# Performance work log

Hardware: AMD Instinct MI355X
Metric: run time of the kernel (lower is better)

Reference implementation:

```python
import jax, jax.numpy as jnp
import numpy as np

N_NODES = 100000
N_EDGES = 1600000
EDGE_FEAT = 16
EDGE_HID = 32
NODE_FEAT = 128


def setup_inputs() -> dict:
    key = jax.random.key(0)
    ks = jax.random.split(key, 10)
    inp = {
        "edge_logits": jax.random.normal(ks[0], (N_EDGES, 1), dtype=jnp.float32),
        "edge_feats": jax.random.normal(ks[1], (N_EDGES, EDGE_FEAT), dtype=jnp.float32),
        "node_feats": jax.random.normal(ks[2], (N_NODES, NODE_FEAT), dtype=jnp.float32),
        "dst": jax.random.randint(ks[3], (N_EDGES,), 0, N_NODES, dtype=jnp.int32),
        # edge_transform Linear(edge_feat -> edge_hid)
        "W_et": jax.random.normal(ks[4], (EDGE_FEAT, EDGE_HID), dtype=jnp.float32) * (1.0 / np.sqrt(EDGE_FEAT)),
        "b_et": jnp.zeros((EDGE_HID,), dtype=jnp.float32),
        # MLP Linear(edge_hid + node_feat -> node_feat)
        "W1": jax.random.normal(ks[5], (EDGE_HID + NODE_FEAT, NODE_FEAT), dtype=jnp.float32) * (1.0 / np.sqrt(EDGE_HID + NODE_FEAT)),
        "b1": jnp.zeros((NODE_FEAT,), dtype=jnp.float32),
        # MLP Linear(node_feat -> node_feat)
        "W2": jax.random.normal(ks[6], (NODE_FEAT, NODE_FEAT), dtype=jnp.float32) * (1.0 / np.sqrt(NODE_FEAT)),
        "b2": jnp.zeros((NODE_FEAT,), dtype=jnp.float32),
    }
    return inp


def reference(edge_logits, edge_feats, node_feats, dst, W_et, b_et, W1, b1, W2, b2):
    # edge_softmax: segment softmax of edge_logits grouped by destination node
    logits = edge_logits[:, 0]                                        # [E]
    seg_max = jax.ops.segment_max(logits, dst, num_segments=N_NODES)  # [N]
    seg_max = jnp.where(jnp.isfinite(seg_max), seg_max, 0.0)          # guard empty segments
    ex = jnp.exp(logits - seg_max[dst])                               # [E]
    denom = jax.ops.segment_sum(ex, dst, num_segments=N_NODES)        # [N]
    denom = jnp.where(denom == 0.0, 1.0, denom)
    alpha = ex / denom[dst]                                           # [E]
    # edge transform (dropout is identity in eval) then weight by attention
    e = alpha[:, None] * (edge_feats @ W_et + b_et)                   # [E, H]
    # scatter-sum aggregation to destination nodes
    c = jax.ops.segment_sum(e, dst, num_segments=N_NODES)             # [N, H]
    context = jax.nn.elu(c)
    h = jnp.concatenate([context, node_feats], axis=1)                # [N, H+F]
    h = jax.nn.relu(h @ W1 + b1)
    return jax.nn.relu(h @ W2 + b2)                                   # [N, F]
```

## Files before the change

### kernel.cpp

```cpp
#include <hip/hip_runtime.h>

#define EF 16
#define EH 32
#define NF 128
#define K1 160
#define HS 168
#define H2S 136

typedef __attribute__((ext_vector_type(8))) short bf16x8;
typedef __attribute__((ext_vector_type(4))) float f32x4;

__device__ __forceinline__ unsigned short f2b(float f) {
  unsigned u = __float_as_uint(f);
  u += 0x7FFFu + ((u >> 16) & 1u);
  return (unsigned short)(u >> 16);
}

__global__ void k_init(unsigned* __restrict__ cnt, int n,
                       const float* __restrict__ W1, const float* __restrict__ W2,
                       unsigned short* __restrict__ w1t, unsigned short* __restrict__ w2t) {
  int i = blockIdx.x * blockDim.x + threadIdx.x;
  if (i < n) cnt[i] = 0u;
  if (i < K1 * NF) {
    int nn = i / K1, k = i % K1;
    w1t[i] = f2b(W1[k * NF + nn]);
  } else if (i < K1 * NF + NF * NF) {
    int j = i - K1 * NF;
    int nn = j / NF, k = j % NF;
    w2t[j] = f2b(W2[k * NF + nn]);
  }
}

__global__ void k_hist(const int* __restrict__ dst, unsigned* __restrict__ cnt, int n_edges) {
  int e = blockIdx.x * blockDim.x + threadIdx.x;
  if (e >= n_edges) return;
  atomicAdd(&cnt[dst[e]], 1u);
}

__global__ void k_scan1(const unsigned* __restrict__ cnt, unsigned* __restrict__ offs,
                        unsigned* __restrict__ bsum, int n) {
  __shared__ unsigned ts[256];
  int t = threadIdx.x;
  int base = blockIdx.x * 1024 + t * 4;
  unsigned v[4];
#pragma unroll
  for (int i = 0; i < 4; ++i) { int idx = base + i; v[i] = (idx < n) ? cnt[idx] : 0u; }
  unsigned run = 0;
#pragma unroll
  for (int i = 0; i < 4; ++i) { unsigned x = v[i]; v[i] = run; run += x; }
  ts[t] = run;
  __syncthreads();
  for (int off = 1; off < 256; off <<= 1) {
    unsigned add = (t >= off) ? ts[t - off] : 0u;
    __syncthreads();
    ts[t] += add;
    __syncthreads();
  }
  unsigned texcl = (t > 0) ? ts[t - 1] : 0u;
  if (t == 255) bsum[blockIdx.x] = ts[255];
#pragma unroll
  for (int i = 0; i < 4; ++i) { int idx = base + i; if (idx < n) offs[idx] = v[i] + texcl; }
}

__global__ void k_scan3(unsigned* __restrict__ offs, unsigned* __restrict__ cursor,
                        const unsigned* __restrict__ bsum, int n, int nb) {
  __shared__ unsigned ts[256];
  int t = threadIdx.x;
  ts[t] = (t < nb) ? bsum[t] : 0u;
  __syncthreads();
  for (int off = 1; off < 256; off <<= 1) {
    unsigned add = (t >= off) ? ts[t - off] : 0u;
    __syncthreads();
    ts[t] += add;
    __syncthreads();
  }
  unsigned add = (blockIdx.x > 0) ? ts[blockIdx.x - 1] : 0u;
  int base = blockIdx.x * 1024 + t * 4;
#pragma unroll
  for (int i = 0; i < 4; ++i) {
    int idx = base + i;
    if (idx < n) { unsigned v = offs[idx] + add; offs[idx] = v; cursor[idx] = v; }
  }
}

__global__ __launch_bounds__(256) void k_perm(
    const int* __restrict__ dst, const float* __restrict__ logits,
    unsigned* __restrict__ cursor, uint2* __restrict__ perm,
    int n_edges, int n_nodes, int chunks) {
  int xcd = blockIdx.x & 7;
  int chunk = blockIdx.x >> 3;
  int lo = (int)((long long)n_nodes * xcd >> 3);
  int hi = (int)((long long)n_nodes * (xcd + 1) >> 3);
  int per = (n_edges + chunks - 1) / chunks;
  int e0 = chunk * per;
  int e1 = min(e0 + per, n_edges);
  for (int e = e0 + (int)threadIdx.x; e < e1; e += 256) {
    int d = __builtin_nontemporal_load(&dst[e]);
    if (d >= lo && d < hi) {
      unsigned slot = atomicAdd(&cursor[d], 1u);
      float ex = __expf(__builtin_nontemporal_load(&logits[e]));
      perm[slot] = make_uint2((unsigned)e, __float_as_uint(ex));
    }
  }
}

__global__ __launch_bounds__(256) void k_gather(
    const uint2* __restrict__ perm, const float* __restrict__ efeat,
    const unsigned* __restrict__ cnt, const unsigned* __restrict__ offs,
    const float* __restrict__ W_et, const float* __restrict__ b_et,
    unsigned short* __restrict__ ctxb, int n_nodes) {
  int node = (int)((blockIdx.x * blockDim.x + threadIdx.x) >> 6);
  if (node >= n_nodes) return;
  int lane = threadIdx.x & 63;
  unsigned start = offs[node];
  unsigned deg = cnt[node];
  int g = lane >> 4, c = lane & 15;
  float a = 0.0f, dsum = 0.0f;
  for (unsigned i = g; i < deg; i += 4) {
    uint2 rec = perm[start + i];
    float ex = __uint_as_float(rec.y);
    float f = efeat[(size_t)rec.x * EF + c];
    a += ex * f;
    dsum += ex;
  }
  a += __shfl_xor(a, 16);      a += __shfl_xor(a, 32);
  dsum += __shfl_xor(dsum, 16); dsum += __shfl_xor(dsum, 32);
  float inv = (deg > 0) ? 1.0f / dsum : 0.0f;
  float S = (deg > 0) ? 1.0f : 0.0f;
  int j = lane & 31;
  float acc = 0.0f;
#pragma unroll
  for (int k = 0; k < 16; ++k) {
    float sk = __shfl(a, k);
    acc += sk * W_et[k * EH + j];
  }
  float cv = acc * inv + S * b_et[j];
  float ctxv = (cv > 0.0f) ? cv : (__expf(cv) - 1.0f);
  if (lane < 32) ctxb[(size_t)node * EH + lane] = f2b(ctxv);
}

__global__ __launch_bounds__(256) void k_node(
    const unsigned short* __restrict__ ctxb, const float* __restrict__ nf,
    const unsigned short* __restrict__ w1t, const unsigned short* __restrict__ w2t,
    const float* __restrict__ b1, const float* __restrict__ b2,
    float* __restrict__ out, int n_nodes) {
  __shared__ __align__(16) unsigned short hA[64 * HS];
  __shared__ __align__(16) unsigned short hB[64 * H2S];
  const int t = threadIdx.x;
  const int w = t >> 6, lane = t & 63;
  const int m = lane & 15, q = lane >> 4;
  int n0 = blockIdx.x * 64;
  if (n0 + 64 > n_nodes) n0 = n_nodes - 64;

  {
    int node = t >> 2, j = (t & 3) * 8;
    *(uint4*)&hA[node * HS + j] = *(const uint4*)&ctxb[(size_t)(n0 + node) * EH + j];
  }
#pragma unroll
  for (int i = 0; i < 8; ++i) {
    int idx = t + 256 * i;
    int node = idx >> 5, j = (idx & 31) * 4;
    float4 v = *(const float4*)&nf[(size_t)(n0 + node) * NF + j];
    unsigned short r[4] = {f2b(v.x), f2b(v.y), f2b(v.z), f2b(v.w)};
    *(uint2*)&hA[node * HS + EH + j] = *(const uint2*)r;
  }
  __syncthreads();

  const int mr = w * 16;
  f32x4 acc[8];
#pragma unroll
  for (int nt = 0; nt < 8; ++nt) acc[nt] = (f32x4){0.f, 0.f, 0.f, 0.f};
  for (int ks = 0; ks < 5; ++ks) {
    bf16x8 a = *(const bf16x8*)&hA[(mr + m) * HS + ks * 32 + q * 8];
#pragma unroll
    for (int nt = 0; nt < 8; ++nt) {
      bf16x8 b = *(const bf16x8*)&w1t[(size_t)(nt * 16 + m) * K1 + ks * 32 + q * 8];
      acc[nt] = __builtin_amdgcn_mfma_f32_16x16x32_bf16(a, b, acc[nt], 0, 0, 0);
    }
  }
#pragma unroll
  for (int nt = 0; nt < 8; ++nt) {
    float bb = b1[nt * 16 + m];
#pragma unroll
    for (int r = 0; r < 4; ++r) {
      float v = fmaxf(acc[nt][r] + bb, 0.0f);
      hB[(mr + q * 4 + r) * H2S + nt * 16 + m] = f2b(v);
    }
  }
  __syncthreads();

  f32x4 ac2[8];
#pragma unroll
  for (int nt = 0; nt < 8; ++nt) ac2[nt] = (f32x4){0.f, 0.f, 0.f, 0.f};
  for (int ks = 0; ks < 4; ++ks) {
    bf16x8 a = *(const bf16x8*)&hB[(mr + m) * H2S + ks * 32 + q * 8];
#pragma unroll
    for (int nt = 0; nt < 8; ++nt) {
      bf16x8 b = *(const bf16x8*)&w2t[(size_t)(nt * 16 + m) * NF + ks * 32 + q * 8];
      ac2[nt] = __builtin_amdgcn_mfma_f32_16x16x32_bf16(a, b, ac2[nt], 0, 0, 0);
    }
  }
#pragma unroll
  for (int nt = 0; nt < 8; ++nt) {
    float bb = b2[nt * 16 + m];
#pragma unroll
    for (int r = 0; r < 4; ++r) {
      out[(size_t)(n0 + mr + q * 4 + r) * NF + nt * 16 + m] = fmaxf(ac2[nt][r] + bb, 0.0f);
    }
  }
}

extern "C" void kernel_launch(void* const* d_in, const int* in_sizes, int n_in,
                              void* d_out, int out_size, void* d_ws, size_t ws_size,
                              hipStream_t stream) {
  const float* edge_logits = (const float*)d_in[0];
  const float* edge_feats  = (const float*)d_in[1];
  const float* node_feats  = (const float*)d_in[2];
  const int*   dst         = (const int*)d_in[3];
  const float* W_et        = (const float*)d_in[4];
  const float* b_et        = (const float*)d_in[5];
  const float* W1          = (const float*)d_in[6];
  const float* b1          = (const float*)d_in[7];
  const float* W2          = (const float*)d_in[8];
  const float* b2          = (const float*)d_in[9];
  float* out = (float*)d_out;

  const int E = in_sizes[0];
  const int n = in_sizes[2] / NF;

  unsigned* cnt    = (unsigned*)d_ws;
  unsigned* offs   = cnt + n;
  unsigned* cursor = offs + n;
  unsigned* bsum   = cursor + n;
  uint2* perm = (uint2*)(((uintptr_t)(bsum + 256) + 255) & ~(uintptr_t)255);
  unsigned short* ctxb = (unsigned short*)(perm + E);
  unsigned short* w1t  = ctxb + (size_t)n * EH;
  unsigned short* w2t  = w1t + NF * K1;

  const int thr = 256;
  const int nscan = (n + 1023) / 1024;
  const int chunks = 256;

  k_init<<<(n + thr - 1) / thr, thr, 0, stream>>>(cnt, n, W1, W2, w1t, w2t);
  k_hist<<<(E + thr - 1) / thr, thr, 0, stream>>>(dst, cnt, E);
  k_scan1<<<nscan, 256, 0, stream>>>(cnt, offs, bsum, n);
  k_scan3<<<nscan, 256, 0, stream>>>(offs, cursor, bsum, n, nscan);
  k_perm<<<chunks * 8, 256, 0, stream>>>(dst, edge_logits, cursor, perm, E, n, chunks);
  k_gather<<<(n * 64 + thr - 1) / thr, thr, 0, stream>>>(perm, edge_feats, cnt, offs,
                                                         W_et, b_et, ctxb, n);
  k_node<<<(n + 63) / 64, 256, 0, stream>>>(ctxb, node_feats, w1t, w2t, b1, b2, out, n);
}
```

Before: 470.7 us.

## Record histogram ranks to drop perm atomics; XCD-aware gather with unrolled loads

The histogram kernel now stores each edge's atomic return value as its rank within its destination bucket. The permutation kernel then computes the slot as offs[d]+rank[e] instead of doing a second atomicAdd on a cursor array, which also removes the cursor array. The gather kernel maps blocks to node ranges per XCD so that perm writes and reads land on the same XCD's L2, and unrolls the edge loop four-way with nontemporal feature loads to raise memory-level parallelism. The cost is an extra 6.4 MB write and read of the rank array.

```diff
diff --git a/kernel.cpp b/kernel.cpp
--- a/kernel.cpp
+++ b/kernel.cpp
@@ -31,10 +31,11 @@
   }
 }
 
-__global__ void k_hist(const int* __restrict__ dst, unsigned* __restrict__ cnt, int n_edges) {
+__global__ void k_hist(const int* __restrict__ dst, unsigned* __restrict__ cnt,
+                       unsigned* __restrict__ rank, int n_edges) {
   int e = blockIdx.x * blockDim.x + threadIdx.x;
   if (e >= n_edges) return;
-  atomicAdd(&cnt[dst[e]], 1u);
+  rank[e] = atomicAdd(&cnt[dst[e]], 1u);
 }
 
 __global__ void k_scan1(const unsigned* __restrict__ cnt, unsigned* __restrict__ offs,
@@ -62,8 +63,8 @@
   for (int i = 0; i < 4; ++i) { int idx = base + i; if (idx < n) offs[idx] = v[i] + texcl; }
 }
 
-__global__ void k_scan3(unsigned* __restrict__ offs, unsigned* __restrict__ cursor,
-                        const unsigned* __restrict__ bsum, int n, int nb) {
+__global__ void k_scan3(unsigned* __restrict__ offs, const unsigned* __restrict__ bsum,
+                        int n, int nb) {
   __shared__ unsigned ts[256];
   int t = threadIdx.x;
   ts[t] = (t < nb) ? bsum[t] : 0u;
@@ -77,28 +78,25 @@
   unsigned add = (blockIdx.x > 0) ? ts[blockIdx.x - 1] : 0u;
   int base = blockIdx.x * 1024 + t * 4;
 #pragma unroll
-  for (int i = 0; i < 4; ++i) {
-    int idx = base + i;
-    if (idx < n) { unsigned v = offs[idx] + add; offs[idx] = v; cursor[idx] = v; }
-  }
+  for (int i = 0; i < 4; ++i) { int idx = base + i; if (idx < n) offs[idx] += add; }
 }
 
 __global__ __launch_bounds__(256) void k_perm(
-    const int* __restrict__ dst, const float* __restrict__ logits,
-    unsigned* __restrict__ cursor, uint2* __restrict__ perm,
-    int n_edges, int n_nodes, int chunks) {
+    const int* __restrict__ dst, const unsigned* __restrict__ rank,
+    const float* __restrict__ logits, const unsigned* __restrict__ offs,
+    uint2* __restrict__ perm, int n_edges, int nps, int n_nodes, int chunks) {
   int xcd = blockIdx.x & 7;
   int chunk = blockIdx.x >> 3;
-  int lo = (int)((long long)n_nodes * xcd >> 3);
-  int hi = (int)((long long)n_nodes * (xcd + 1) >> 3);
+  int lo = xcd * nps;
+  int hi = min(lo + nps, n_nodes);
   int per = (n_edges + chunks - 1) / chunks;
   int e0 = chunk * per;
   int e1 = min(e0 + per, n_edges);
   for (int e = e0 + (int)threadIdx.x; e < e1; e += 256) {
-    int d = __builtin_nontemporal_load(&dst[e]);
+    int d = dst[e];
     if (d >= lo && d < hi) {
-      unsigned slot = atomicAdd(&cursor[d], 1u);
-      float ex = __expf(__builtin_nontemporal_load(&logits[e]));
+      unsigned slot = offs[d] + rank[e];
+      float ex = __expf(logits[e]);
       perm[slot] = make_uint2((unsigned)e, __float_as_uint(ex));
     }
   }
@@ -108,18 +106,36 @@
     const uint2* __restrict__ perm, const float* __restrict__ efeat,
     const unsigned* __restrict__ cnt, const unsigned* __restrict__ offs,
     const float* __restrict__ W_et, const float* __restrict__ b_et,
-    unsigned short* __restrict__ ctxb, int n_nodes) {
-  int node = (int)((blockIdx.x * blockDim.x + threadIdx.x) >> 6);
-  if (node >= n_nodes) return;
+    unsigned short* __restrict__ ctxb, int nps, int n_nodes) {
+  int slot4 = blockIdx.x & 7;
+  int idx = blockIdx.x >> 3;
+  int node = slot4 * nps + (idx << 2) + (int)(threadIdx.x >> 6);
+  int slot_end = min(slot4 * nps + nps, n_nodes);
+  if (node >= slot_end) return;
   int lane = threadIdx.x & 63;
   unsigned start = offs[node];
   unsigned deg = cnt[node];
   int g = lane >> 4, c = lane & 15;
   float a = 0.0f, dsum = 0.0f;
-  for (unsigned i = g; i < deg; i += 4) {
+  unsigned i = g;
+  for (; i + 12 < deg; i += 16) {
+    uint2 r0 = perm[start + i];
+    uint2 r1 = perm[start + i + 4];
+    uint2 r2 = perm[start + i + 8];
+    uint2 r3 = perm[start + i + 12];
+    float f0 = __builtin_nontemporal_load(&efeat[(size_t)r0.x * EF + c]);
+    float f1 = __builtin_nontemporal_load(&efeat[(size_t)r1.x * EF + c]);
+    float f2 = __builtin_nontemporal_load(&efeat[(size_t)r2.x * EF + c]);
+    float f3 = __builtin_nontemporal_load(&efeat[(size_t)r3.x * EF + c]);
+    float e0 = __uint_as_float(r0.y), e1 = __uint_as_float(r1.y);
+    float e2 = __uint_as_float(r2.y), e3 = __uint_as_float(r3.y);
+    a += e0 * f0 + e1 * f1 + e2 * f2 + e3 * f3;
+    dsum += (e0 + e1) + (e2 + e3);
+  }
+  for (; i < deg; i += 4) {
     uint2 rec = perm[start + i];
     float ex = __uint_as_float(rec.y);
-    float f = efeat[(size_t)rec.x * EF + c];
+    float f = __builtin_nontemporal_load(&efeat[(size_t)rec.x * EF + c]);
     a += ex * f;
     dsum += ex;
   }
@@ -228,11 +244,11 @@
   const int E = in_sizes[0];
   const int n = in_sizes[2] / NF;
 
-  unsigned* cnt    = (unsigned*)d_ws;
-  unsigned* offs   = cnt + n;
-  unsigned* cursor = offs + n;
-  unsigned* bsum   = cursor + n;
-  uint2* perm = (uint2*)(((uintptr_t)(bsum + 256) + 255) & ~(uintptr_t)255);
+  unsigned* cnt  = (unsigned*)d_ws;
+  unsigned* offs = cnt + n;
+  unsigned* bsum = offs + n;
+  unsigned* rank = bsum + 256;
+  uint2* perm = (uint2*)(((uintptr_t)(rank + E) + 255) & ~(uintptr_t)255);
   unsigned short* ctxb = (unsigned short*)(perm + E);
   unsigned short* w1t  = ctxb + (size_t)n * EH;
   unsigned short* w2t  = w1t + NF * K1;
@@ -240,13 +256,14 @@
   const int thr = 256;
   const int nscan = (n + 1023) / 1024;
   const int chunks = 256;
+  const int nps = (n + 7) >> 3;
 
   k_init<<<(n + thr - 1) / thr, thr, 0, stream>>>(cnt, n, W1, W2, w1t, w2t);
-  k_hist<<<(E + thr - 1) / thr, thr, 0, stream>>>(dst, cnt, E);
+  k_hist<<<(E + thr - 1) / thr, thr, 0, stream>>>(dst, cnt, rank, E);
   k_scan1<<<nscan, 256, 0, stream>>>(cnt, offs, bsum, n);
-  k_scan3<<<nscan, 256, 0, stream>>>(offs, cursor, bsum, n, nscan);
-  k_perm<<<chunks * 8, 256, 0, stream>>>(dst, edge_logits, cursor, perm, E, n, chunks);
-  k_gather<<<(n * 64 + thr - 1) / thr, thr, 0, stream>>>(perm, edge_feats, cnt, offs,
-                                                         W_et, b_et, ctxb, n);
+  k_scan3<<<nscan, 256, 0, stream>>>(offs, bsum, n, nscan);
+  k_perm<<<chunks * 8, 256, 0, stream>>>(dst, rank, edge_logits, offs, perm, E, nps, n, chunks);
+  const int gblocks = 8 * ((nps + 3) >> 2);
+  k_gather<<<gblocks, 256, 0, stream>>>(perm, edge_feats, cnt, offs, W_et, b_et, ctxb, nps, n);
   k_node<<<(n + 63) / 64, 256, 0, stream>>>(ctxb, node_feats, w1t, w2t, b1, b2, out, n);
 }
```

Result: faster. 430.6 us (-8.5%).
